# Kernel tuning notes

Hardware: AMD Instinct MI355X
Metric: run time of the kernel (lower is better)

## Reference

```python
import jax, jax.numpy as jnp
import numpy as np

DIM = 64  # module-level global `dim` used as the softmax scale


def setup_inputs() -> dict:
    key = jax.random.key(0)
    kq, kk, kv, km = jax.random.split(key, 4)
    B, H, S, d = 4, 16, 2048, DIM
    Q = jax.random.normal(kq, (B, H, S, d), dtype=jnp.float32)
    K = jax.random.normal(kk, (B, H, S, d), dtype=jnp.float32)
    V = jax.random.normal(kv, (B, H, S, d), dtype=jnp.float32)
    attn_mask = jax.random.randint(km, (B, H, S, S), 0, 2).astype(jnp.bool_)
    return {"Q": Q, "K": K, "V": V, "attn_mask": attn_mask}


def reference(Q, K, V, attn_mask):
    scale = 1.0 / np.sqrt(DIM).astype(np.float32)
    # scores: [B, H, S, S]
    scores = jnp.einsum("bhqd,bhkd->bhqk", Q, K) * scale
    # NOTE: original torch code does masked_fill_(attn_mask, 0) — fills with 0, not -inf
    scores = jnp.where(attn_mask, jnp.zeros((), scores.dtype), scores)
    attn = jax.nn.softmax(scores, axis=-1)
    context = jnp.einsum("bhqk,bhkd->bhqd", attn, V)
    return context
```

## Files before the change

kernel.cpp:

```cpp
#include <hip/hip_runtime.h>
#include <hip/hip_bf16.h>

typedef __bf16 bf16;
typedef __attribute__((ext_vector_type(8))) __bf16 bf16x8;
typedef __attribute__((ext_vector_type(4))) __bf16 bf16x4;
typedef __attribute__((ext_vector_type(4))) float f32x4;
typedef __attribute__((ext_vector_type(4))) int i32x4;

constexpr int SLEN = 2048;
constexpr int DH = 64;
constexpr int NBH = 64;
constexpr float SCALE_LOG2E = 0.125f * 1.4426950408889634f;

__global__ void cast_k_kernel(const float* __restrict__ in, bf16* __restrict__ out) {
    size_t i = (size_t)blockIdx.x * blockDim.x + threadIdx.x;
    const float4* p = (const float4*)in + i * 2;
    float4 a = p[0], b = p[1];
    bf16x8 v;
    v[0]=(bf16)a.x; v[1]=(bf16)a.y; v[2]=(bf16)a.z; v[3]=(bf16)a.w;
    v[4]=(bf16)b.x; v[5]=(bf16)b.y; v[6]=(bf16)b.z; v[7]=(bf16)b.w;
    ((bf16x8*)out)[i] = v;
}

__global__ void transpose_v_kernel(const float* __restrict__ V, bf16* __restrict__ Vt) {
    __shared__ float t[64][65];
    int bh = blockIdx.y;
    int s0 = blockIdx.x * 64;
    int tx = threadIdx.x & 63, ty = threadIdx.x >> 6;
    const float* vp = V + ((size_t)bh * SLEN + s0) * DH;
    #pragma unroll
    for (int r = ty; r < 64; r += 4) t[r][tx] = vp[(size_t)r * DH + tx];
    __syncthreads();
    bf16* op = Vt + (size_t)bh * DH * SLEN + s0;
    #pragma unroll
    for (int r = ty; r < 64; r += 4) op[(size_t)r * SLEN + tx] = (bf16)t[tx][r];
}

__device__ __forceinline__ void gl_lds16(const void* g, void* l) {
    __builtin_amdgcn_global_load_lds(
        (const __attribute__((address_space(1))) void*)g,
        (__attribute__((address_space(3))) void*)l, 16, 0, 0);
}

__global__ __launch_bounds__(256) void attn_kernel(
    const float* __restrict__ Q, const int* __restrict__ mask,
    const bf16* __restrict__ Kb, const bf16* __restrict__ Vtb,
    float* __restrict__ out)
{
    __shared__ char KT[2][8192];
    __shared__ char VT[2][8192];
    __shared__ char MT[2][16384];
    __shared__ bf16 P_lds[64][72];

    const int bh = blockIdx.y;
    const int qbase = blockIdx.x * 64;
    const int tid = threadIdx.x;
    const int w = tid >> 6, l = tid & 63;
    const int lq = l & 15, lg = l >> 4;

    const char* kgb = (const char*)(Kb + (size_t)bh * SLEN * DH);
    const char* vgb = (const char*)(Vtb + (size_t)bh * DH * SLEN);
    const char* mgb = (const char*)(mask + ((size_t)bh * SLEN + qbase) * SLEN);

    const int kv_r = l >> 3;
    const int kv_c = ((l & 7) * 16) ^ (kv_r << 4);

    bf16x8 aq[2];
    {
        const float* qp = Q + ((size_t)bh * SLEN + qbase + w * 16 + lq) * DH + lg * 8;
        #pragma unroll
        for (int t = 0; t < 2; ++t) {
            float4 x = *(const float4*)(qp + t * 32);
            float4 y = *(const float4*)(qp + t * 32 + 4);
            bf16x8 f;
            f[0]=(bf16)x.x; f[1]=(bf16)x.y; f[2]=(bf16)x.z; f[3]=(bf16)x.w;
            f[4]=(bf16)y.x; f[5]=(bf16)y.y; f[6]=(bf16)y.z; f[7]=(bf16)y.w;
            aq[t] = f;
        }
    }

    f32x4 acc[4] = {{0,0,0,0},{0,0,0,0},{0,0,0,0},{0,0,0,0}};
    float dpart = 0.f;
    const int swzk = (lq & 7) << 4;

    auto stage = [&](int kb, int buf) {
        #pragma unroll
        for (int q = 0; q < 2; ++q) {
            int r = (w * 2 + q) * 8 + kv_r;
            gl_lds16(kgb + (size_t)(kb + r) * 128 + kv_c,
                     &KT[buf][(w * 2 + q) * 1024]);
            gl_lds16(vgb + (size_t)r * 4096 + (size_t)kb * 2 + kv_c,
                     &VT[buf][(w * 2 + q) * 1024]);
        }
        #pragma unroll
        for (int q = 0; q < 4; ++q) {
            int r = (w * 4 + q) * 4 + (l >> 4);
            int c = ((l & 15) * 16) ^ ((r & 15) << 4);
            gl_lds16(mgb + (size_t)r * 8192 + (size_t)kb * 4 + c,
                     &MT[buf][(w * 4 + q) * 1024]);
        }
    };

    stage(0, 0);
    __syncthreads();

    int cur = 0;
    for (int kt = 0; kt < SLEN / 64; ++kt) {
        if (kt + 1 < SLEN / 64) stage((kt + 1) * 64, cur ^ 1);

        #pragma unroll
        for (int n = 0; n < 4; ++n) {
            f32x4 s = {0, 0, 0, 0};
            #pragma unroll
            for (int t = 0; t < 2; ++t) {
                bf16x8 bk = *(const bf16x8*)&KT[cur][(n * 16 + lq) * 128 + ((t * 64 + lg * 16) ^ swzk)];
                s = __builtin_amdgcn_mfma_f32_16x16x32_bf16(bk, aq[t], s, 0, 0, 0);
            }
            i32x4 mv = *(const i32x4*)&MT[cur][(w * 16 + lq) * 256 + ((n * 64 + lg * 16) ^ (lq << 4))];
            bf16x4 pk;
            #pragma unroll
            for (int i = 0; i < 4; ++i) {
                float e = mv[i] ? 0.0f : s[i] * SCALE_LOG2E;
                float p = exp2f(e);
                dpart += p;
                pk[i] = (bf16)p;
            }
            *(bf16x4*)(&P_lds[w * 16 + lq][n * 16 + lg * 4]) = pk;
        }

        #pragma unroll
        for (int n = 0; n < 4; ++n) {
            #pragma unroll
            for (int kk = 0; kk < 2; ++kk) {
                bf16x8 ap = *(const bf16x8*)(&P_lds[w * 16 + lq][kk * 32 + lg * 8]);
                bf16x8 bv = *(const bf16x8*)&VT[cur][(n * 16 + lq) * 128 + ((kk * 64 + lg * 16) ^ swzk)];
                acc[n] = __builtin_amdgcn_mfma_f32_16x16x32_bf16(ap, bv, acc[n], 0, 0, 0);
            }
        }

        __syncthreads();
        cur ^= 1;
    }

    dpart += __shfl_xor(dpart, 16, 64);
    dpart += __shfl_xor(dpart, 32, 64);
    float dinv = 1.0f / dpart;

    float di[4];
    #pragma unroll
    for (int i = 0; i < 4; ++i) di[i] = __shfl(dinv, lg * 4 + i, 64);

    float* op = out + ((size_t)bh * SLEN + qbase + w * 16) * DH;
    #pragma unroll
    for (int n = 0; n < 4; ++n) {
        #pragma unroll
        for (int i = 0; i < 4; ++i)
            op[(size_t)(lg * 4 + i) * DH + n * 16 + lq] = acc[n][i] * di[i];
    }
}

extern "C" void kernel_launch(void* const* d_in, const int* in_sizes, int n_in,
                              void* d_out, int out_size, void* d_ws, size_t ws_size,
                              hipStream_t stream) {
    const float* Q    = (const float*)d_in[0];
    const float* K    = (const float*)d_in[1];
    const float* V    = (const float*)d_in[2];
    const int*   mask = (const int*)d_in[3];
    float* out = (float*)d_out;

    bf16* Kb  = (bf16*)d_ws;
    bf16* Vtb = Kb + (size_t)NBH * SLEN * DH;

    int n8 = NBH * SLEN * DH / 8;
    cast_k_kernel<<<n8 / 256, 256, 0, stream>>>(K, Kb);
    transpose_v_kernel<<<dim3(SLEN / 64, NBH), 256, 0, stream>>>(V, Vtb);
    attn_kernel<<<dim3(SLEN / 64, NBH), 256, 0, stream>>>(Q, mask, Kb, Vtb, out);
}
```

Measured before the change: 371.6 us.

## Load mask directly into registers with nontemporal prefetch, shrink LDS footprint

Mask tiles are no longer staged through LDS. Each lane now reads its own mask values straight into registers with nontemporal loads and prefetches the next tile one iteration ahead. The P scratch buffer becomes a compact XOR-swizzled 8 KB tile instead of a padded array, and launch bounds ask for 4 blocks per CU. Together these cut LDS use so more blocks can be resident, and they keep the large streaming mask out of the caches. In exchange the mask loads become per-lane register loads that are less coalesced, and register pressure rises from the prefetch buffers.

Measured after the change: 323.2 us. 1.15x faster.

```diff
diff --git a/kernel.cpp b/kernel.cpp
--- a/kernel.cpp
+++ b/kernel.cpp
@@ -42,15 +42,14 @@
         (__attribute__((address_space(3))) void*)l, 16, 0, 0);
 }
 
-__global__ __launch_bounds__(256) void attn_kernel(
+__global__ __launch_bounds__(256, 4) void attn_kernel(
     const float* __restrict__ Q, const int* __restrict__ mask,
     const bf16* __restrict__ Kb, const bf16* __restrict__ Vtb,
     float* __restrict__ out)
 {
     __shared__ char KT[2][8192];
     __shared__ char VT[2][8192];
-    __shared__ char MT[2][16384];
-    __shared__ bf16 P_lds[64][72];
+    __shared__ char PT[8192];
 
     const int bh = blockIdx.y;
     const int qbase = blockIdx.x * 64;
@@ -60,7 +59,6 @@
 
     const char* kgb = (const char*)(Kb + (size_t)bh * SLEN * DH);
     const char* vgb = (const char*)(Vtb + (size_t)bh * DH * SLEN);
-    const char* mgb = (const char*)(mask + ((size_t)bh * SLEN + qbase) * SLEN);
 
     const int kv_r = l >> 3;
     const int kv_c = ((l & 7) * 16) ^ (kv_r << 4);
@@ -82,31 +80,38 @@
     f32x4 acc[4] = {{0,0,0,0},{0,0,0,0},{0,0,0,0},{0,0,0,0}};
     float dpart = 0.f;
     const int swzk = (lq & 7) << 4;
+    const int prow = w * 16 + lq;
+    char* pb = PT + prow * 128;
+    const int pswz = (prow & 7) << 4;
 
     auto stage = [&](int kb, int buf) {
         #pragma unroll
         for (int q = 0; q < 2; ++q) {
             int r = (w * 2 + q) * 8 + kv_r;
-            gl_lds16(kgb + (size_t)(kb + r) * 128 + kv_c,
-                     &KT[buf][(w * 2 + q) * 1024]);
-            gl_lds16(vgb + (size_t)r * 4096 + (size_t)kb * 2 + kv_c,
-                     &VT[buf][(w * 2 + q) * 1024]);
-        }
-        #pragma unroll
-        for (int q = 0; q < 4; ++q) {
-            int r = (w * 4 + q) * 4 + (l >> 4);
-            int c = ((l & 15) * 16) ^ ((r & 15) << 4);
-            gl_lds16(mgb + (size_t)r * 8192 + (size_t)kb * 4 + c,
-                     &MT[buf][(w * 4 + q) * 1024]);
+            gl_lds16(kgb + (size_t)(kb + r) * 128 + kv_c, &KT[buf][(w * 2 + q) * 1024]);
+            gl_lds16(vgb + (size_t)r * 4096 + (size_t)kb * 2 + kv_c, &VT[buf][(w * 2 + q) * 1024]);
         }
     };
+
+    const int* mrow = mask + ((size_t)bh * SLEN + qbase + w * 16 + lq) * SLEN;
+    i32x4 mcur[4], mnext[4];
+    #pragma unroll
+    for (int n = 0; n < 4; ++n)
+        mcur[n] = __builtin_nontemporal_load((const i32x4*)(mrow + n * 16 + lg * 4));
 
     stage(0, 0);
     __syncthreads();
 
     int cur = 0;
     for (int kt = 0; kt < SLEN / 64; ++kt) {
-        if (kt + 1 < SLEN / 64) stage((kt + 1) * 64, cur ^ 1);
+        const bool has_next = (kt + 1) < (SLEN / 64);
+        if (has_next) {
+            stage((kt + 1) * 64, cur ^ 1);
+            #pragma unroll
+            for (int n = 0; n < 4; ++n)
+                mnext[n] = __builtin_nontemporal_load(
+                    (const i32x4*)(mrow + (kt + 1) * 64 + n * 16 + lg * 4));
+        }
 
         #pragma unroll
         for (int n = 0; n < 4; ++n) {
@@ -116,28 +121,31 @@
                 bf16x8 bk = *(const bf16x8*)&KT[cur][(n * 16 + lq) * 128 + ((t * 64 + lg * 16) ^ swzk)];
                 s = __builtin_amdgcn_mfma_f32_16x16x32_bf16(bk, aq[t], s, 0, 0, 0);
             }
-            i32x4 mv = *(const i32x4*)&MT[cur][(w * 16 + lq) * 256 + ((n * 64 + lg * 16) ^ (lq << 4))];
             bf16x4 pk;
             #pragma unroll
             for (int i = 0; i < 4; ++i) {
-                float e = mv[i] ? 0.0f : s[i] * SCALE_LOG2E;
+                float e = mcur[n][i] ? 0.0f : s[i] * SCALE_LOG2E;
                 float p = exp2f(e);
                 dpart += p;
                 pk[i] = (bf16)p;
             }
-            *(bf16x4*)(&P_lds[w * 16 + lq][n * 16 + lg * 4]) = pk;
+            *(bf16x4*)(pb + ((n * 32 + lg * 8) ^ pswz)) = pk;
         }
 
         #pragma unroll
         for (int n = 0; n < 4; ++n) {
             #pragma unroll
             for (int kk = 0; kk < 2; ++kk) {
-                bf16x8 ap = *(const bf16x8*)(&P_lds[w * 16 + lq][kk * 32 + lg * 8]);
+                bf16x8 ap = *(const bf16x8*)(pb + ((kk * 64 + lg * 16) ^ pswz));
                 bf16x8 bv = *(const bf16x8*)&VT[cur][(n * 16 + lq) * 128 + ((kk * 64 + lg * 16) ^ swzk)];
                 acc[n] = __builtin_amdgcn_mfma_f32_16x16x32_bf16(ap, bv, acc[n], 0, 0, 0);
             }
         }
 
+        if (has_next) {
+            #pragma unroll
+            for (int n = 0; n < 4; ++n) mcur[n] = mnext[n];
+        }
         __syncthreads();
         cur ^= 1;
     }
```
